# Kernel optimization log

Hardware: AMD Instinct MI355X
Metric: run time of the kernel (lower is better)

The kernel has to match this reference:

```python
import jax, jax.numpy as jnp
import numpy as np

N_NODES = 64
HIDDEN = 16
SCALE = HIDDEN ** -0.5
NEG_INF = -1e9


def setup_inputs() -> dict:
    key = jax.random.key(0)
    ks = jax.random.split(key, 5)
    x = jax.random.normal(ks[0], (256, 1, N_NODES, 4096), dtype=jnp.float32)
    wq = jax.random.normal(ks[1], (HIDDEN,), dtype=jnp.float32)
    bq = jax.random.normal(ks[2], (HIDDEN,), dtype=jnp.float32)
    wk = jax.random.normal(ks[3], (HIDDEN,), dtype=jnp.float32)
    bk = jax.random.normal(ks[4], (HIDDEN,), dtype=jnp.float32)
    return {"x": x, "wq": wq, "bq": bq, "wk": wk, "bk": bk}


def reference(x, wq, bq, wk, bk):
    xs = x[:, 0]                                   # (B, 64, T)
    # torch.var defaults to unbiased (ddof=1)
    e = jnp.var(xs, axis=-1, ddof=1)               # (B, 64)
    # Conv1d(1, H, k=1) == per-channel affine: (B, H, 64)
    Q = wq[None, :, None] * e[:, None, :] + bq[None, :, None]
    K = wk[None, :, None] * e[:, None, :] + bk[None, :, None]
    attn = jnp.einsum('bhi,bhj->bij', Q, K) * SCALE  # (B, 64, 64)
    eye = jnp.eye(N_NODES, dtype=bool)
    attn = jnp.where(eye[None], NEG_INF, attn)
    attn_weights = jax.nn.softmax(attn, axis=-1)
    out = jnp.einsum('bij,bjt->bit', attn_weights, xs)  # (B, 64, T)
    return out[:, None] + x, attn_weights
```

## Files before the change

### kernel.cpp

```cpp
#include <hip/hip_runtime.h>

#define NB 256
#define NN 64
#define NT 4096

__global__ __launch_bounds__(256) void var_kernel(const float* __restrict__ x,
                                                  float* __restrict__ e) {
    int row = blockIdx.x;
    const float4* xr = (const float4*)(x + (size_t)row * NT);
    int tid = threadIdx.x;
    float s = 0.f, ss = 0.f;
#pragma unroll
    for (int k = 0; k < 4; ++k) {
        float4 v = xr[tid + k * 256];
        s  += (v.x + v.y) + (v.z + v.w);
        ss += (v.x * v.x + v.y * v.y) + (v.z * v.z + v.w * v.w);
    }
#pragma unroll
    for (int off = 32; off > 0; off >>= 1) {
        s  += __shfl_down(s, off);
        ss += __shfl_down(ss, off);
    }
    __shared__ float sh[8];
    int w = tid >> 6;
    if ((tid & 63) == 0) { sh[w] = s; sh[4 + w] = ss; }
    __syncthreads();
    if (tid == 0) {
        float S  = (sh[0] + sh[1]) + (sh[2] + sh[3]);
        float SS = (sh[4] + sh[5]) + (sh[6] + sh[7]);
        float mean = S * (1.0f / NT);
        e[row] = (SS - (float)NT * mean * mean) * (1.0f / (NT - 1));
    }
}

__global__ __launch_bounds__(64) void attn_kernel(const float* __restrict__ e,
                                                  const float* __restrict__ wq,
                                                  const float* __restrict__ bq,
                                                  const float* __restrict__ wk,
                                                  const float* __restrict__ bk,
                                                  float* __restrict__ attn_out,
                                                  float* __restrict__ wprime) {
    int b = blockIdx.x;
    int i = threadIdx.x;
    float A = 0.f, Bq = 0.f, Bk = 0.f, C = 0.f;
#pragma unroll
    for (int h = 0; h < 16; ++h) {
        A  += wq[h] * wk[h];
        Bq += wq[h] * bk[h];
        Bk += bq[h] * wk[h];
        C  += bq[h] * bk[h];
    }
    __shared__ float es[NN];
    es[i] = e[b * NN + i];
    __syncthreads();
    float ei = es[i];
    float l[NN];
    float m = -3.0e38f;
#pragma unroll
    for (int j = 0; j < NN; ++j) {
        float v = 0.25f * (A * ei * es[j] + Bq * ei + Bk * es[j] + C);
        if (j == i) v = -1.0e9f;
        l[j] = v;
        m = fmaxf(m, v);
    }
    float sum = 0.f;
#pragma unroll
    for (int j = 0; j < NN; ++j) {
        float ev = expf(l[j] - m);
        l[j] = ev;
        sum += ev;
    }
    float inv = 1.0f / sum;
    float* dst = attn_out + (size_t)b * (NN * NN) + i * NN;
    float* wp  = wprime   + (size_t)b * (NN * NN) + i * NN;
#pragma unroll
    for (int j = 0; j < NN; ++j) {
        float w = l[j] * inv;
        dst[j] = w;
        wp[j]  = (j == i) ? 1.0f : w;
    }
}

__global__ __launch_bounds__(128) void out_kernel(const float* __restrict__ x,
                                                  const float* __restrict__ Wp,
                                                  float* __restrict__ out) {
    int blk = blockIdx.x;
    int b = blk >> 5;
    int chunk = blk & 31;
    int t = chunk * 128 + threadIdx.x;
    const float* xb = x + (size_t)b * (NN * NT) + t;

    float xv[NN];
#pragma unroll
    for (int j = 0; j < NN; ++j) xv[j] = xb[(size_t)j * NT];

    const float* Wb = Wp + (size_t)b * (NN * NN);
    float* ob = out + (size_t)b * (NN * NT) + t;

#pragma unroll 1
    for (int i = 0; i < NN; i += 4) {
        const float* W0 = Wb + (i + 0) * NN;
        const float* W1 = Wb + (i + 1) * NN;
        const float* W2 = Wb + (i + 2) * NN;
        const float* W3 = Wb + (i + 3) * NN;
        float a0 = 0.f, a1 = 0.f, a2 = 0.f, a3 = 0.f;
#pragma unroll
        for (int j = 0; j < NN; ++j) {
            float v = xv[j];
            a0 = fmaf(W0[j], v, a0);
            a1 = fmaf(W1[j], v, a1);
            a2 = fmaf(W2[j], v, a2);
            a3 = fmaf(W3[j], v, a3);
        }
        ob[(size_t)(i + 0) * NT] = a0;
        ob[(size_t)(i + 1) * NT] = a1;
        ob[(size_t)(i + 2) * NT] = a2;
        ob[(size_t)(i + 3) * NT] = a3;
    }
}

extern "C" void kernel_launch(void* const* d_in, const int* in_sizes, int n_in,
                              void* d_out, int out_size, void* d_ws, size_t ws_size,
                              hipStream_t stream) {
    const float* x  = (const float*)d_in[0];
    const float* wq = (const float*)d_in[1];
    const float* bq = (const float*)d_in[2];
    const float* wk = (const float*)d_in[3];
    const float* bk = (const float*)d_in[4];
    float* out  = (float*)d_out;
    float* attn = out + (size_t)NB * NN * NT;
    float* e    = (float*)d_ws;
    float* wp   = (float*)d_ws + NB * NN;

    var_kernel<<<NB * NN, 256, 0, stream>>>(x, e);
    attn_kernel<<<NB, 64, 0, stream>>>(e, wq, bq, wk, bk, attn, wp);
    out_kernel<<<NB * 32, 128, 0, stream>>>(x, wp, out);
}
```

Before: 576.3 us.

## Restructure output GEMM to outer-product accumulation with transposed weights, warp-per-row variance

The output kernel now streams one x row at a time and accumulates all 64 output rows in registers, using a transposed weight matrix written by the attention kernel, instead of holding all 64 x values and looping over output rows. Blocks grow to 256 threads covering 256 time steps each. The variance kernel assigns one wavefront per row so each block reduces four rows with shuffles only, removing the shared-memory step and block barrier. The transposed weight stores in the attention kernel are strided and uncoalesced, and 64 accumulators plus a 2x unroll raise register pressure, which may reduce occupancy.

```diff
diff --git a/kernel.cpp b/kernel.cpp
--- a/kernel.cpp
+++ b/kernel.cpp
@@ -6,13 +6,13 @@
 
 __global__ __launch_bounds__(256) void var_kernel(const float* __restrict__ x,
                                                   float* __restrict__ e) {
-    int row = blockIdx.x;
+    int row  = blockIdx.x * 4 + (threadIdx.x >> 6);
+    int lane = threadIdx.x & 63;
     const float4* xr = (const float4*)(x + (size_t)row * NT);
-    int tid = threadIdx.x;
     float s = 0.f, ss = 0.f;
 #pragma unroll
-    for (int k = 0; k < 4; ++k) {
-        float4 v = xr[tid + k * 256];
+    for (int k = 0; k < 16; ++k) {
+        float4 v = xr[lane + k * 64];
         s  += (v.x + v.y) + (v.z + v.w);
         ss += (v.x * v.x + v.y * v.y) + (v.z * v.z + v.w * v.w);
     }
@@ -21,15 +21,9 @@
         s  += __shfl_down(s, off);
         ss += __shfl_down(ss, off);
     }
-    __shared__ float sh[8];
-    int w = tid >> 6;
-    if ((tid & 63) == 0) { sh[w] = s; sh[4 + w] = ss; }
-    __syncthreads();
-    if (tid == 0) {
-        float S  = (sh[0] + sh[1]) + (sh[2] + sh[3]);
-        float SS = (sh[4] + sh[5]) + (sh[6] + sh[7]);
-        float mean = S * (1.0f / NT);
-        e[row] = (SS - (float)NT * mean * mean) * (1.0f / (NT - 1));
+    if (lane == 0) {
+        float mean = s * (1.0f / NT);
+        e[row] = (ss - (float)NT * mean * mean) * (1.0f / (NT - 1));
     }
 }
 
@@ -39,7 +33,7 @@
                                                   const float* __restrict__ wk,
                                                   const float* __restrict__ bk,
                                                   float* __restrict__ attn_out,
-                                                  float* __restrict__ wprime) {
+                                                  float* __restrict__ wpT) {
     int b = blockIdx.x;
     int i = threadIdx.x;
     float A = 0.f, Bq = 0.f, Bk = 0.f, C = 0.f;
@@ -72,51 +66,39 @@
     }
     float inv = 1.0f / sum;
     float* dst = attn_out + (size_t)b * (NN * NN) + i * NN;
-    float* wp  = wprime   + (size_t)b * (NN * NN) + i * NN;
+    float* wt  = wpT      + (size_t)b * (NN * NN);
 #pragma unroll
     for (int j = 0; j < NN; ++j) {
         float w = l[j] * inv;
         dst[j] = w;
-        wp[j]  = (j == i) ? 1.0f : w;
+        wt[j * NN + i] = (j == i) ? 1.0f : w;
     }
 }
 
-__global__ __launch_bounds__(128) void out_kernel(const float* __restrict__ x,
-                                                  const float* __restrict__ Wp,
+__global__ __launch_bounds__(256) void out_kernel(const float* __restrict__ x,
+                                                  const float* __restrict__ WpT,
                                                   float* __restrict__ out) {
     int blk = blockIdx.x;
-    int b = blk >> 5;
-    int chunk = blk & 31;
-    int t = chunk * 128 + threadIdx.x;
+    int b = blk >> 4;
+    int t = (blk & 15) * 256 + threadIdx.x;
     const float* xb = x + (size_t)b * (NN * NT) + t;
+    const float* Wb = WpT + (size_t)b * (NN * NN);
 
-    float xv[NN];
+    float acc[NN];
 #pragma unroll
-    for (int j = 0; j < NN; ++j) xv[j] = xb[(size_t)j * NT];
+    for (int i = 0; i < NN; ++i) acc[i] = 0.f;
 
-    const float* Wb = Wp + (size_t)b * (NN * NN);
+#pragma unroll 2
+    for (int j = 0; j < NN; ++j) {
+        float xv = xb[(size_t)j * NT];
+        const float* Wr = Wb + j * NN;
+#pragma unroll
+        for (int i = 0; i < NN; ++i) acc[i] = fmaf(Wr[i], xv, acc[i]);
+    }
+
     float* ob = out + (size_t)b * (NN * NT) + t;
-
-#pragma unroll 1
-    for (int i = 0; i < NN; i += 4) {
-        const float* W0 = Wb + (i + 0) * NN;
-        const float* W1 = Wb + (i + 1) * NN;
-        const float* W2 = Wb + (i + 2) * NN;
-        const float* W3 = Wb + (i + 3) * NN;
-        float a0 = 0.f, a1 = 0.f, a2 = 0.f, a3 = 0.f;
 #pragma unroll
-        for (int j = 0; j < NN; ++j) {
-            float v = xv[j];
-            a0 = fmaf(W0[j], v, a0);
-            a1 = fmaf(W1[j], v, a1);
-            a2 = fmaf(W2[j], v, a2);
-            a3 = fmaf(W3[j], v, a3);
-        }
-        ob[(size_t)(i + 0) * NT] = a0;
-        ob[(size_t)(i + 1) * NT] = a1;
-        ob[(size_t)(i + 2) * NT] = a2;
-        ob[(size_t)(i + 3) * NT] = a3;
-    }
+    for (int i = 0; i < NN; ++i) ob[(size_t)i * NT] = acc[i];
 }
 
 extern "C" void kernel_launch(void* const* d_in, const int* in_sizes, int n_in,
@@ -130,9 +112,9 @@
     float* out  = (float*)d_out;
     float* attn = out + (size_t)NB * NN * NT;
     float* e    = (float*)d_ws;
-    float* wp   = (float*)d_ws + NB * NN;
+    float* wpT  = (float*)d_ws + NB * NN;
 
-    var_kernel<<<NB * NN, 256, 0, stream>>>(x, e);
-    attn_kernel<<<NB, 64, 0, stream>>>(e, wq, bq, wk, bk, attn, wp);
-    out_kernel<<<NB * 32, 128, 0, stream>>>(x, wp, out);
+    var_kernel<<<NB * NN / 4, 256, 0, stream>>>(x, e);
+    attn_kernel<<<NB, 64, 0, stream>>>(e, wq, bq, wk, bk, attn, wpT);
+    out_kernel<<<NB * 16, 256, 0, stream>>>(x, wpT, out);
 }
```

Result: no change. 575.7 us (-0.1%).
